# Kernel optimization log

Measured on AMD Instinct MI355X. Metric: run time of the kernel, lower is better.

The kernel has to match this reference:

```python
import jax, jax.numpy as jnp
import numpy as np

D_MODEL = 1024

def setup_inputs() -> dict:
    key = jax.random.key(0)
    ks = jax.random.split(key, 7)
    s = 1.0 / np.sqrt(D_MODEL)
    x = jax.random.normal(ks[0], (4, 2048, D_MODEL), dtype=jnp.float32)
    wq_w = jax.random.uniform(ks[1], (D_MODEL, D_MODEL), jnp.float32, -s, s)
    wq_b = jax.random.uniform(ks[2], (D_MODEL,), jnp.float32, -s, s)
    wk_w = jax.random.uniform(ks[3], (D_MODEL, D_MODEL), jnp.float32, -s, s)
    wk_b = jax.random.uniform(ks[4], (D_MODEL,), jnp.float32, -s, s)
    wv_w = jax.random.uniform(ks[5], (D_MODEL, D_MODEL), jnp.float32, -s, s)
    wv_b = jax.random.uniform(ks[6], (D_MODEL,), jnp.float32, -s, s)
    return {"x": x, "wq_w": wq_w, "wq_b": wq_b, "wk_w": wk_w, "wk_b": wk_b, "wv_w": wv_w, "wv_b": wv_b}

def reference(x, wq_w, wq_b, wk_w, wk_b, wv_w, wv_b):
    # Linear: x @ W^T + b (torch nn.Linear convention)
    q = jnp.einsum('bsd,ed->bse', x, wq_w) + wq_b
    k = jnp.einsum('bsd,ed->bse', x, wk_w) + wk_b
    v = jnp.einsum('bsd,ed->bse', x, wv_w) + wv_b
    scale = 1.0 / jnp.sqrt(jnp.asarray(k.shape[-1], dtype=q.dtype))
    logits = jnp.einsum('bqd,bkd->bqk', q, k) * scale  # [B, S, S]
    attn = jax.nn.softmax(logits, axis=-1)
    out = jnp.einsum('bqk,bkd->bqd', attn, v)
    return (attn, out)
```

## Files before the change

kernel.cpp:

```cpp
#include <hip/hip_runtime.h>

typedef unsigned short u16;
typedef u16 u16x4 __attribute__((ext_vector_type(4)));
typedef u16 u16x8 __attribute__((ext_vector_type(8)));
typedef __bf16 bf16x8 __attribute__((ext_vector_type(8)));
typedef float f32x4 __attribute__((ext_vector_type(4)));
typedef float f32x16 __attribute__((ext_vector_type(16)));

static __device__ __forceinline__ u16 f2bf(float f) {
  unsigned u = __builtin_bit_cast(unsigned, f);
  u += 0x7fffu + ((u >> 16) & 1u);
  return (u16)(u >> 16);
}
static __device__ __forceinline__ float bf2f(u16 h) {
  return __builtin_bit_cast(float, ((unsigned)h) << 16);
}

static __device__ __forceinline__ void gload_lds16(const u16* g, u16* l) {
  u16* gn = const_cast<u16*>(g);
  __builtin_amdgcn_global_load_lds(
      (__attribute__((address_space(1))) unsigned int*)gn,
      (__attribute__((address_space(3))) unsigned int*)l,
      16, 0, 0);
}

__global__ __launch_bounds__(256)
void cvt_f32_bf16(const float* __restrict__ in, u16* __restrict__ out) {
  const int i = blockIdx.x * 256 + threadIdx.x;
  float4 f = ((const float4*)in)[i];
  u16x4 o = { f2bf(f.x), f2bf(f.y), f2bf(f.z), f2bf(f.w) };
  ((u16x4*)out)[i] = o;
}

__global__ __launch_bounds__(256)
void cvt_w3(const float* __restrict__ a, const float* __restrict__ b,
            const float* __restrict__ c, u16* __restrict__ out) {
  const int blk = blockIdx.x;
  const int w = blk >> 10;
  const float* src = (w == 0) ? a : (w == 1) ? b : c;
  const int i = (blk & 1023) * 256 + threadIdx.x;
  float4 f = ((const float4*)src)[i];
  u16x4 o = { f2bf(f.x), f2bf(f.y), f2bf(f.z), f2bf(f.w) };
  ((u16x4*)(out + (size_t)w * 1048576ULL))[i] = o;
}


#define MM16(a, b, c) __builtin_amdgcn_mfma_f32_16x16x32_bf16(a, b, c, 0, 0, 0)

#define STAGE_A(BUF, J, KT) \
  gload_lds16(Ag + (size_t)(J) * 32 * lda + (KT), AsW + (BUF) * 16384 + (J) * 2048)
#define STAGE_B(BUF, KS, RH, KT) \
  gload_lds16(Bg + (size_t)(RH) * 32 * ldb + (KS) * 32 + (KT), \
              BsW + (BUF) * 16384 + (KS) * 2048 + (RH) * 1024)

#define APTR(BUF, MI, KS) \
  ((const bf16x8*)(ArdBase + (BUF) * 16384 + (MI) * 1024 + ((pA0 ^ ((KS) << 2)) << 3)))
#define BPTR(BUF, NI, KS) \
  ((const bf16x8*)(BrdBase + (BUF) * 16384 + (KS) * 2048 + (NI) * 512))

#define RD8(S, BUF, MH, KS) \
    S##A0 = *APTR(BUF, (MH) * 4 + 0, KS); \
    S##A1 = *APTR(BUF, (MH) * 4 + 1, KS); \
    S##A2 = *APTR(BUF, (MH) * 4 + 2, KS); \
    S##A3 = *APTR(BUF, (MH) * 4 + 3, KS); \
    S##B0 = *BPTR(BUF, 0, KS); \
    S##B1 = *BPTR(BUF, 1, KS); \
    S##B2 = *BPTR(BUF, 2, KS); \
    S##B3 = *BPTR(BUF, 3, KS)

#define PH(CUR, NXT, MH, NBUF, NMH, NKS, STG) do {                          \
    RD8(NXT, NBUF, NMH, NKS);                                               \
    STG;                                                                    \
    __builtin_amdgcn_s_barrier();                                           \
    asm volatile("s_waitcnt lgkmcnt(8)" ::: "memory");                      \
    __builtin_amdgcn_sched_barrier(0);                                      \
    __builtin_amdgcn_s_setprio(1);                                          \
    acc[(MH)*4+0][0] = MM16(CUR##A0, CUR##B0, acc[(MH)*4+0][0]);            \
    acc[(MH)*4+1][0] = MM16(CUR##A1, CUR##B0, acc[(MH)*4+1][0]);            \
    acc[(MH)*4+2][0] = MM16(CUR##A2, CUR##B0, acc[(MH)*4+2][0]);            \
    acc[(MH)*4+3][0] = MM16(CUR##A3, CUR##B0, acc[(MH)*4+3][0]);            \
    acc[(MH)*4+0][1] = MM16(CUR##A0, CUR##B1, acc[(MH)*4+0][1]);            \
    acc[(MH)*4+1][1] = MM16(CUR##A1, CUR##B1, acc[(MH)*4+1][1]);            \
    acc[(MH)*4+2][1] = MM16(CUR##A2, CUR##B1, acc[(MH)*4+2][1]);            \
    acc[(MH)*4+3][1] = MM16(CUR##A3, CUR##B1, acc[(MH)*4+3][1]);            \
    acc[(MH)*4+0][2] = MM16(CUR##A0, CUR##B2, acc[(MH)*4+0][2]);            \
    acc[(MH)*4+1][2] = MM16(CUR##A1, CUR##B2, acc[(MH)*4+1][2]);            \
    acc[(MH)*4+2][2] = MM16(CUR##A2, CUR##B2, acc[(MH)*4+2][2]);            \
    acc[(MH)*4+3][2] = MM16(CUR##A3, CUR##B2, acc[(MH)*4+3][2]);            \
    acc[(MH)*4+0][3] = MM16(CUR##A0, CUR##B3, acc[(MH)*4+0][3]);            \
    acc[(MH)*4+1][3] = MM16(CUR##A1, CUR##B3, acc[(MH)*4+1][3]);            \
    acc[(MH)*4+2][3] = MM16(CUR##A2, CUR##B3, acc[(MH)*4+2][3]);            \
    acc[(MH)*4+3][3] = MM16(CUR##A3, CUR##B3, acc[(MH)*4+3][3]);            \
    __builtin_amdgcn_s_setprio(0);                                          \
    asm volatile("s_waitcnt vmcnt(2)" ::: "memory");                        \
    __builtin_amdgcn_sched_barrier(0);                                      \
    __builtin_amdgcn_s_barrier();                                           \
  } while (0)

template<int MODE>
__global__ __launch_bounds__(512, 2)
void gemm8p(const u16* __restrict__ Ain, const u16* __restrict__ Bin,
            void* __restrict__ Cv,
            const float* __restrict__ b0, const float* __restrict__ b1,
            const float* __restrict__ b2,
            int lda, int ldb, int ldc, int K,
            unsigned long long sA, unsigned long long sB, unsigned long long sC,
            int nbx, int nby)
{
  __shared__ alignas(16) u16 As[2 * 2 * 128 * 64];
  __shared__ alignas(16) u16 Bs[2 * 4 * 2 * 64 * 32];

  const int nbxy = nbx * nby;
  const int bid  = blockIdx.x;
  const int flat = (bid & 7) * ((int)gridDim.x >> 3) + (bid >> 3);
  const int z    = flat / nbxy;
  const int rr   = flat - z * nbxy;
  const int width = nbx << 3;
  const int gid  = rr / width;
  const int rw   = rr - gid * width;
  const int by   = (gid << 3) + (rw & 7);
  const int bx   = rw >> 3;

  const u16* A = Ain + z * sA;
  const u16* B = Bin + z * sB;

  const int tid  = threadIdx.x;
  const int wave = tid >> 6;
  const int lane = tid & 63;
  const int wr   = wave >> 2;
  const int wc   = wave & 3;
  const int l16  = lane & 15;
  const int l4   = lane >> 4;

  const int m0 = by << 8;
  const int n0 = bx << 8;

  const int asr = wc * 8 + (lane >> 3);
  const int asc = ((lane & 7) ^ (lane >> 3)) << 3;
  const u16* Ag = A + (size_t)(m0 + wr * 128 + asr) * lda + asc;
  u16* AsW = As + wr * 8192 + wc * 512;

  const int bsr = wr * 16 + (lane >> 2);
  const int bsc = ((lane & 3) ^ ((lane >> 3) & 3)) << 3;
  const u16* Bg = B + (size_t)(n0 + wc * 64 + bsr) * ldb + bsc;
  u16* BsW = Bs + wc * 4096 + wr * 512;

  const u16* ArdBase = As + (wr * 128 + l16) * 64;
  const int pA0 = l4 ^ (l16 & 7);
  const u16* BrdBase = Bs + wc * 4096 + l16 * 32 + ((l4 ^ ((l16 >> 1) & 3)) << 3);

  f32x4 acc[8][4];
  #pragma unroll
  for (int i = 0; i < 8; ++i)
    #pragma unroll
    for (int j = 0; j < 4; ++j)
      #pragma unroll
      for (int r = 0; r < 4; ++r)
        acc[i][j][r] = 0.f;

  bf16x8 xA0, xA1, xA2, xA3, xB0, xB1, xB2, xB3;
  bf16x8 yA0, yA1, yA2, yA3, yB0, yB1, yB2, yB3;

  STAGE_A(0, 0, 0); STAGE_A(0, 1, 0);
  STAGE_B(0, 0, 0, 0); STAGE_B(0, 0, 1, 0);
  STAGE_B(0, 1, 0, 0); STAGE_B(0, 1, 1, 0);
  STAGE_A(0, 2, 0); STAGE_A(0, 3, 0);
  asm volatile("s_waitcnt vmcnt(0)" ::: "memory");
  __builtin_amdgcn_sched_barrier(0);
  __builtin_amdgcn_s_barrier();
  RD8(x, 0, 0, 0);

  const int NT = K >> 6;
  for (int t = 0; t < NT; t += 2) {
    const int k1 = (t + 1) * 64;
    const int k2 = (t + 2 < NT) ? (t + 2) * 64 : 0;
    PH(x, y, 0, 0, 0, 1, STAGE_A(1, 0, k1); STAGE_A(1, 1, k1));
    PH(y, x, 0, 0, 1, 0, STAGE_B(1, 0, 0, k1); STAGE_B(1, 0, 1, k1));
    PH(x, y, 1, 0, 1, 1, STAGE_B(1, 1, 0, k1); STAGE_B(1, 1, 1, k1));
    PH(y, x, 1, 1, 0, 0, STAGE_A(1, 2, k1); STAGE_A(1, 3, k1));
    PH(x, y, 0, 1, 0, 1, STAGE_A(0, 0, k2); STAGE_A(0, 1, k2));
    PH(y, x, 0, 1, 1, 0, STAGE_B(0, 0, 0, k2); STAGE_B(0, 0, 1, k2));
    PH(x, y, 1, 1, 1, 1, STAGE_B(0, 1, 0, k2); STAGE_B(0, 1, 1, k2));
    PH(y, x, 1, 0, 0, 0, STAGE_A(0, 2, k2); STAGE_A(0, 3, k2));
  }
  asm volatile("s_waitcnt vmcnt(0)" ::: "memory");

  if constexpr (MODE == 0) {
    const int g = n0 >> 10;
    const int colb = (n0 + wc * 64) & 1023;
    const int rowb = m0 + wr * 128 + l4 * 4;
    if (g < 2) {
      u16* Cb = (u16*)Cv + (size_t)g * 8388608ULL;
      const float* bp = (g == 0) ? b0 : b1;
      const float qs = (g == 0) ? 0.03125f : 1.0f;
      #pragma unroll
      for (int ni = 0; ni < 4; ++ni) {
        const int col = colb + ni * 16 + l16;
        const float bv = bp[col];
        #pragma unroll
        for (int mi = 0; mi < 8; ++mi) {
          const int row = rowb + mi * 16;
          #pragma unroll
          for (int r = 0; r < 4; ++r)
            Cb[(size_t)(row + r) * 1024 + col] = f2bf((acc[mi][ni][r] + bv) * qs);
        }
      }
    } else {
      u16* Vt = (u16*)Cv + 16777216ULL;
      #pragma unroll
      for (int ni = 0; ni < 4; ++ni) {
        const int col = colb + ni * 16 + l16;
        const float bv = b2[col];
        #pragma unroll
        for (int mi = 0; mi < 8; ++mi) {
          const int row = rowb + mi * 16;
          u16x4 o;
          #pragma unroll
          for (int r = 0; r < 4; ++r) o[r] = f2bf(acc[mi][ni][r] + bv);
          const size_t idx = ((size_t)((row >> 11) * 1024 + col)) * 2048 + (row & 2047);
          *(u16x4*)&Vt[idx] = o;
        }
      }
    }
  } else {
    u16* Cb = (u16*)Cv + (size_t)z * sC;
    #pragma unroll
    for (int ni = 0; ni < 4; ++ni) {
      const int col = n0 + wc * 64 + ni * 16 + l16;
      #pragma unroll
      for (int mi = 0; mi < 8; ++mi) {
        const int row = m0 + wr * 128 + mi * 16 + l4 * 4;
        #pragma unroll
        for (int r = 0; r < 4; ++r)
          Cb[(size_t)(row + r) * ldc + col] = f2bf(acc[mi][ni][r]);
      }
    }
  }
}

template<int MODE>
__global__ __launch_bounds__(256)
void gemm_bt(const u16* __restrict__ Ain, const u16* __restrict__ Bin,
             void* __restrict__ Cv,
             const float* __restrict__ b0, const float* __restrict__ b1,
             const float* __restrict__ b2,
             int lda, int ldb, int ldc, int K,
             unsigned long long sA, unsigned long long sB, unsigned long long sC,
             int nbx, int nby)
{
  constexpr int BM = 128, BN = 128, BK = 64;
  __shared__ alignas(16) u16 As[BM * BK];
  __shared__ alignas(16) u16 Bs[BN * BK];

  const int nbxy = nbx * nby;
  const int bid  = blockIdx.x;
  const int flat = (bid & 7) * ((int)gridDim.x >> 3) + (bid >> 3);
  const int z    = flat / nbxy;
  const int rr   = flat - z * nbxy;
  const int width = nbx << 3;
  const int gid  = rr / width;
  const int rw   = rr - gid * width;
  const int by   = (gid << 3) + (rw & 7);
  const int bx   = rw >> 3;

  const u16* A = Ain + z * sA;
  const u16* B = Bin + z * sB;

  const int tid  = threadIdx.x;
  const int wave = tid >> 6;
  const int lane = tid & 63;
  const int l32  = lane & 31;
  const int half = lane >> 5;
  const int wr   = wave >> 1;
  const int wc   = wave & 1;

  const int m0 = by * BM;
  const int n0 = bx * BN;

  const int lr = lane >> 3;
  const int sc = ((lane & 7) ^ lr) * 8;
  const u16* Ag = A + (size_t)(m0 + wave * 32 + lr) * lda + sc;
  const u16* Bg = B + (size_t)(n0 + wave * 32 + lr) * ldb + sc;
  u16* Asb = &As[(wave * 32) * BK];
  u16* Bsb = &Bs[(wave * 32) * BK];

  f32x16 acc[2][2];
  #pragma unroll
  for (int i = 0; i < 2; ++i)
    #pragma unroll
    for (int j = 0; j < 2; ++j)
      #pragma unroll
      for (int r = 0; r < 16; ++r)
        acc[i][j][r] = 0.f;

  for (int k0 = 0; k0 < K; k0 += BK) {
    gload_lds16(Ag + k0,                    Asb);
    gload_lds16(Ag + (size_t) 8 * lda + k0, Asb +  8 * BK);
    gload_lds16(Ag + (size_t)16 * lda + k0, Asb + 16 * BK);
    gload_lds16(Ag + (size_t)24 * lda + k0, Asb + 24 * BK);
    gload_lds16(Bg + k0,                    Bsb);
    gload_lds16(Bg + (size_t) 8 * ldb + k0, Bsb +  8 * BK);
    gload_lds16(Bg + (size_t)16 * ldb + k0, Bsb + 16 * BK);
    gload_lds16(Bg + (size_t)24 * ldb + k0, Bsb + 24 * BK);
    __syncthreads();

    #pragma unroll
    for (int ks = 0; ks < 4; ++ks) {
      bf16x8 af[2], bfr[2];
      #pragma unroll
      for (int ti = 0; ti < 2; ++ti) {
        const int row = wr * 64 + ti * 32 + l32;
        const int ch  = ((ks * 2 + half) ^ (row & 7)) * 8;
        af[ti] = *(const bf16x8*)&As[row * BK + ch];
      }
      #pragma unroll
      for (int tj = 0; tj < 2; ++tj) {
        const int row = wc * 64 + tj * 32 + l32;
        const int ch  = ((ks * 2 + half) ^ (row & 7)) * 8;
        bfr[tj] = *(const bf16x8*)&Bs[row * BK + ch];
      }
      #pragma unroll
      for (int ti = 0; ti < 2; ++ti)
        #pragma unroll
        for (int tj = 0; tj < 2; ++tj)
          acc[ti][tj] = __builtin_amdgcn_mfma_f32_32x32x16_bf16(af[ti], bfr[tj], acc[ti][tj], 0, 0, 0);
    }
    __syncthreads();
  }

  const int colb = n0 + wc * 64 + l32;
  const int rowb = m0 + wr * 64 + 4 * half;

  if constexpr (MODE == 3) {
    float* Cf = (float*)Cv + z * sC;
    #pragma unroll
    for (int tj = 0; tj < 2; ++tj) {
      const int col = colb + tj * 32;
      #pragma unroll
      for (int ti = 0; ti < 2; ++ti)
        #pragma unroll
        for (int g4 = 0; g4 < 4; ++g4)
          #pragma unroll
          for (int r = 0; r < 4; ++r) {
            const int row = rowb + ti * 32 + g4 * 8 + r;
            Cf[(size_t)row * ldc + col] = acc[ti][tj][g4 * 4 + r];
          }
    }
  }
}

__global__ __launch_bounds__(256)
void softmax_rows(u16* __restrict__ logits, float* __restrict__ attn) {
  const int row = blockIdx.x;
  const int tid = threadIdx.x;
  u16*   lp = logits + (size_t)row * 2048 + tid * 8;
  float* ap = attn   + (size_t)row * 2048 + tid * 8;

  u16x8 raw = *(const u16x8*)lp;
  float v[8];
  #pragma unroll
  for (int j = 0; j < 8; ++j) v[j] = bf2f(raw[j]);

  float mx = v[0];
  #pragma unroll
  for (int j = 1; j < 8; ++j) mx = fmaxf(mx, v[j]);
  #pragma unroll
  for (int o = 32; o > 0; o >>= 1) mx = fmaxf(mx, __shfl_xor(mx, o, 64));

  __shared__ float smax[4], ssum[4];
  const int wv = tid >> 6, ln = tid & 63;
  if (ln == 0) smax[wv] = mx;
  __syncthreads();
  mx = fmaxf(fmaxf(smax[0], smax[1]), fmaxf(smax[2], smax[3]));

  float s = 0.f;
  #pragma unroll
  for (int j = 0; j < 8; ++j) { v[j] = __expf(v[j] - mx); s += v[j]; }
  #pragma unroll
  for (int o = 32; o > 0; o >>= 1) s += __shfl_xor(s, o, 64);
  if (ln == 0) ssum[wv] = s;
  __syncthreads();
  s = (ssum[0] + ssum[1]) + (ssum[2] + ssum[3]);
  const float inv = 1.f / s;

  u16x8 ob;
  #pragma unroll
  for (int j = 0; j < 8; ++j) { v[j] *= inv; ob[j] = f2bf(v[j]); }
  float4* apv = (float4*)ap;
  apv[0] = make_float4(v[0], v[1], v[2], v[3]);
  apv[1] = make_float4(v[4], v[5], v[6], v[7]);
  *(u16x8*)lp = ob;
}

extern "C" void kernel_launch(void* const* d_in, const int* in_sizes, int n_in,
                              void* d_out, int out_size, void* d_ws, size_t ws_size,
                              hipStream_t stream) {
  (void)in_sizes; (void)n_in; (void)out_size; (void)ws_size;
  const float* x    = (const float*)d_in[0];
  const float* wq_w = (const float*)d_in[1];
  const float* wq_b = (const float*)d_in[2];
  const float* wk_w = (const float*)d_in[3];
  const float* wk_b = (const float*)d_in[4];
  const float* wv_w = (const float*)d_in[5];
  const float* wv_b = (const float*)d_in[6];

  float* attn = (float*)d_out;
  float* outp = attn + 16777216ULL;

  u16* xb   = (u16*)d_ws;
  u16* wcat = xb   + 8388608ULL;
  u16* Qb   = wcat + 3145728ULL;
  u16* Kb   = Qb   + 8388608ULL;
  u16* Vt   = Kb   + 8388608ULL;
  u16* Lg   = Vt   + 8388608ULL;

  cvt_f32_bf16<<<8192, 256, 0, stream>>>(x, xb);
  cvt_w3<<<3072, 256, 0, stream>>>(wq_w, wk_w, wv_w, wcat);

  gemm8p<0><<<384, 512, 0, stream>>>(xb, wcat, Qb, wq_b, wk_b, wv_b,
                                     1024, 1024, 1024, 1024, 0, 0, 0, 12, 32);

  gemm8p<2><<<256, 512, 0, stream>>>(Qb, Kb, Lg, nullptr, nullptr, nullptr,
                                     1024, 1024, 2048, 1024,
                                     2097152ULL, 2097152ULL, 4194304ULL, 8, 8);

  softmax_rows<<<8192, 256, 0, stream>>>(Lg, attn);

  gemm_bt<3><<<512, 256, 0, stream>>>(Lg, Vt, outp, nullptr, nullptr, nullptr,
                                      2048, 2048, 1024, 2048,
                                      4194304ULL, 2097152ULL, 2097152ULL, 8, 16);
}
```

Before: 332.0 us.

## Restructure gemm8p LDS staging into k-half tiles with deeper prefetch and B-register reuse

Reworks the 256x256 GEMM pipeline. Shared-memory tiles are now split into two 32-wide k-halves for both A and B, with a single swizzle pattern. Loads are issued one k-tile further ahead, with vmcnt waits only every fourth phase, and B fragments are read once and reused across the two M-halves instead of being re-read per phase. The cost is waiting for all LDS reads (lgkmcnt(0)) before each MFMA batch, which drops the previous register double-buffering, and launch bounds drop to one block per CU. The gemm_bt signature also loses its unused bias pointers.

```diff
diff --git a/kernel.cpp b/kernel.cpp
--- a/kernel.cpp
+++ b/kernel.cpp
@@ -47,58 +47,67 @@
 
 #define MM16(a, b, c) __builtin_amdgcn_mfma_f32_16x16x32_bf16(a, b, c, 0, 0, 0)
 
-#define STAGE_A(BUF, J, KT) \
-  gload_lds16(Ag + (size_t)(J) * 32 * lda + (KT), AsW + (BUF) * 16384 + (J) * 2048)
-#define STAGE_B(BUF, KS, RH, KT) \
-  gload_lds16(Bg + (size_t)(RH) * 32 * ldb + (KS) * 32 + (KT), \
-              BsW + (BUF) * 16384 + (KS) * 2048 + (RH) * 1024)
+#define STAGE_A(BUF, KH, KT) do {                                            \
+    gload_lds16(Asrc + (KT) + (KH) * 32,                                     \
+                AsW + (BUF) * 16384 + (KH) * 8192);                          \
+    gload_lds16(Asrc + (size_t)128 * lda + (KT) + (KH) * 32,                 \
+                AsW + (BUF) * 16384 + (KH) * 8192 + 4096);                   \
+  } while (0)
+#define STAGE_B(BUF, KH, KT) do {                                            \
+    gload_lds16(Bsrc + (KT) + (KH) * 32,                                     \
+                BsW + (BUF) * 16384 + (KH) * 8192);                          \
+    gload_lds16(Bsrc + (size_t)128 * ldb + (KT) + (KH) * 32,                 \
+                BsW + (BUF) * 16384 + (KH) * 8192 + 4096);                   \
+  } while (0)
 
 #define APTR(BUF, MI, KS) \
-  ((const bf16x8*)(ArdBase + (BUF) * 16384 + (MI) * 1024 + ((pA0 ^ ((KS) << 2)) << 3)))
+  ((const bf16x8*)(ArdBase + (BUF) * 16384 + (KS) * 8192 + (MI) * 512))
 #define BPTR(BUF, NI, KS) \
-  ((const bf16x8*)(BrdBase + (BUF) * 16384 + (KS) * 2048 + (NI) * 512))
-
-#define RD8(S, BUF, MH, KS) \
-    S##A0 = *APTR(BUF, (MH) * 4 + 0, KS); \
-    S##A1 = *APTR(BUF, (MH) * 4 + 1, KS); \
-    S##A2 = *APTR(BUF, (MH) * 4 + 2, KS); \
-    S##A3 = *APTR(BUF, (MH) * 4 + 3, KS); \
-    S##B0 = *BPTR(BUF, 0, KS); \
-    S##B1 = *BPTR(BUF, 1, KS); \
-    S##B2 = *BPTR(BUF, 2, KS); \
-    S##B3 = *BPTR(BUF, 3, KS)
-
-#define PH(CUR, NXT, MH, NBUF, NMH, NKS, STG) do {                          \
-    RD8(NXT, NBUF, NMH, NKS);                                               \
-    STG;                                                                    \
-    __builtin_amdgcn_s_barrier();                                           \
-    asm volatile("s_waitcnt lgkmcnt(8)" ::: "memory");                      \
-    __builtin_amdgcn_sched_barrier(0);                                      \
-    __builtin_amdgcn_s_setprio(1);                                          \
-    acc[(MH)*4+0][0] = MM16(CUR##A0, CUR##B0, acc[(MH)*4+0][0]);            \
-    acc[(MH)*4+1][0] = MM16(CUR##A1, CUR##B0, acc[(MH)*4+1][0]);            \
-    acc[(MH)*4+2][0] = MM16(CUR##A2, CUR##B0, acc[(MH)*4+2][0]);            \
-    acc[(MH)*4+3][0] = MM16(CUR##A3, CUR##B0, acc[(MH)*4+3][0]);            \
-    acc[(MH)*4+0][1] = MM16(CUR##A0, CUR##B1, acc[(MH)*4+0][1]);            \
-    acc[(MH)*4+1][1] = MM16(CUR##A1, CUR##B1, acc[(MH)*4+1][1]);            \
-    acc[(MH)*4+2][1] = MM16(CUR##A2, CUR##B1, acc[(MH)*4+2][1]);            \
-    acc[(MH)*4+3][1] = MM16(CUR##A3, CUR##B1, acc[(MH)*4+3][1]);            \
-    acc[(MH)*4+0][2] = MM16(CUR##A0, CUR##B2, acc[(MH)*4+0][2]);            \
-    acc[(MH)*4+1][2] = MM16(CUR##A1, CUR##B2, acc[(MH)*4+1][2]);            \
-    acc[(MH)*4+2][2] = MM16(CUR##A2, CUR##B2, acc[(MH)*4+2][2]);            \
-    acc[(MH)*4+3][2] = MM16(CUR##A3, CUR##B2, acc[(MH)*4+3][2]);            \
-    acc[(MH)*4+0][3] = MM16(CUR##A0, CUR##B3, acc[(MH)*4+0][3]);            \
-    acc[(MH)*4+1][3] = MM16(CUR##A1, CUR##B3, acc[(MH)*4+1][3]);            \
-    acc[(MH)*4+2][3] = MM16(CUR##A2, CUR##B3, acc[(MH)*4+2][3]);            \
-    acc[(MH)*4+3][3] = MM16(CUR##A3, CUR##B3, acc[(MH)*4+3][3]);            \
-    __builtin_amdgcn_s_setprio(0);                                          \
-    asm volatile("s_waitcnt vmcnt(2)" ::: "memory");                        \
-    __builtin_amdgcn_sched_barrier(0);                                      \
-    __builtin_amdgcn_s_barrier();                                           \
+  ((const bf16x8*)(BrdBase + (BUF) * 16384 + (KS) * 8192 + (NI) * 512))
+
+#define VM4   asm volatile("s_waitcnt vmcnt(4)" ::: "memory")
+#define NOVM  (void)0
+
+#define PH(BUF, MH, KS, RDB, STG, VMW) do {                                  \
+    bf16x8 a0 = *APTR(BUF, (MH) * 4 + 0, KS);                                \
+    bf16x8 a1 = *APTR(BUF, (MH) * 4 + 1, KS);                                \
+    bf16x8 a2 = *APTR(BUF, (MH) * 4 + 2, KS);                                \
+    bf16x8 a3 = *APTR(BUF, (MH) * 4 + 3, KS);                                \
+    if (RDB) {                                                               \
+      bf0 = *BPTR(BUF, 0, KS);                                               \
+      bf1 = *BPTR(BUF, 1, KS);                                               \
+      bf2 = *BPTR(BUF, 2, KS);                                               \
+      bf3 = *BPTR(BUF, 3, KS);                                               \
+    }                                                                        \
+    STG;                                                                     \
+    __builtin_amdgcn_s_barrier();                                            \
+    asm volatile("s_waitcnt lgkmcnt(0)" ::: "memory");                       \
+    __builtin_amdgcn_sched_barrier(0);                                       \
+    __builtin_amdgcn_s_setprio(1);                                           \
+    acc[(MH)*4+0][0] = MM16(a0, bf0, acc[(MH)*4+0][0]);                      \
+    acc[(MH)*4+1][0] = MM16(a1, bf0, acc[(MH)*4+1][0]);                      \
+    acc[(MH)*4+2][0] = MM16(a2, bf0, acc[(MH)*4+2][0]);                      \
+    acc[(MH)*4+3][0] = MM16(a3, bf0, acc[(MH)*4+3][0]);                      \
+    acc[(MH)*4+0][1] = MM16(a0, bf1, acc[(MH)*4+0][1]);                      \
+    acc[(MH)*4+1][1] = MM16(a1, bf1, acc[(MH)*4+1][1]);                      \
+    acc[(MH)*4+2][1] = MM16(a2, bf1, acc[(MH)*4+2][1]);                      \
+    acc[(MH)*4+3][1] = MM16(a3, bf1, acc[(MH)*4+3][1]);                      \
+    acc[(MH)*4+0][2] = MM16(a0, bf2, acc[(MH)*4+0][2]);                      \
+    acc[(MH)*4+1][2] = MM16(a1, bf2, acc[(MH)*4+1][2]);                      \
+    acc[(MH)*4+2][2] = MM16(a2, bf2, acc[(MH)*4+2][2]);                      \
+    acc[(MH)*4+3][2] = MM16(a3, bf2, acc[(MH)*4+3][2]);                      \
+    acc[(MH)*4+0][3] = MM16(a0, bf3, acc[(MH)*4+0][3]);                      \
+    acc[(MH)*4+1][3] = MM16(a1, bf3, acc[(MH)*4+1][3]);                      \
+    acc[(MH)*4+2][3] = MM16(a2, bf3, acc[(MH)*4+2][3]);                      \
+    acc[(MH)*4+3][3] = MM16(a3, bf3, acc[(MH)*4+3][3]);                      \
+    __builtin_amdgcn_s_setprio(0);                                           \
+    VMW;                                                                     \
+    __builtin_amdgcn_sched_barrier(0);                                       \
+    __builtin_amdgcn_s_barrier();                                            \
   } while (0)
 
 template<int MODE>
-__global__ __launch_bounds__(512, 2)
+__global__ __launch_bounds__(512, 1)
 void gemm8p(const u16* __restrict__ Ain, const u16* __restrict__ Bin,
             void* __restrict__ Cv,
             const float* __restrict__ b0, const float* __restrict__ b1,
@@ -107,8 +116,8 @@
             unsigned long long sA, unsigned long long sB, unsigned long long sC,
             int nbx, int nby)
 {
-  __shared__ alignas(16) u16 As[2 * 2 * 128 * 64];
-  __shared__ alignas(16) u16 Bs[2 * 4 * 2 * 64 * 32];
+  __shared__ alignas(16) u16 As[2 * 2 * 256 * 32];
+  __shared__ alignas(16) u16 Bs[2 * 2 * 256 * 32];
 
   const int nbxy = nbx * nby;
   const int bid  = blockIdx.x;
@@ -135,19 +144,15 @@
   const int m0 = by << 8;
   const int n0 = bx << 8;
 
-  const int asr = wc * 8 + (lane >> 3);
-  const int asc = ((lane & 7) ^ (lane >> 3)) << 3;
-  const u16* Ag = A + (size_t)(m0 + wr * 128 + asr) * lda + asc;
-  u16* AsW = As + wr * 8192 + wc * 512;
-
-  const int bsr = wr * 16 + (lane >> 2);
-  const int bsc = ((lane & 3) ^ ((lane >> 3) & 3)) << 3;
-  const u16* Bg = B + (size_t)(n0 + wc * 64 + bsr) * ldb + bsc;
-  u16* BsW = Bs + wc * 4096 + wr * 512;
-
-  const u16* ArdBase = As + (wr * 128 + l16) * 64;
-  const int pA0 = l4 ^ (l16 & 7);
-  const u16* BrdBase = Bs + wc * 4096 + l16 * 32 + ((l4 ^ ((l16 >> 1) & 3)) << 3);
+  const int gch = (tid & 3) ^ ((tid >> 3) & 3);
+  const u16* Asrc = A + (size_t)(m0 + (tid >> 2)) * lda + gch * 8;
+  const u16* Bsrc = B + (size_t)(n0 + (tid >> 2)) * ldb + gch * 8;
+  u16* AsW = As + tid * 8;
+  u16* BsW = Bs + tid * 8;
+
+  const int rsw = (l4 ^ ((l16 >> 1) & 3)) << 3;
+  const u16* ArdBase = As + (size_t)(wr * 128 + l16) * 32 + rsw;
+  const u16* BrdBase = Bs + (size_t)(wc * 64 + l16) * 32 + rsw;
 
   f32x4 acc[8][4];
   #pragma unroll
@@ -158,30 +163,28 @@
       for (int r = 0; r < 4; ++r)
         acc[i][j][r] = 0.f;
 
-  bf16x8 xA0, xA1, xA2, xA3, xB0, xB1, xB2, xB3;
-  bf16x8 yA0, yA1, yA2, yA3, yB0, yB1, yB2, yB3;
-
-  STAGE_A(0, 0, 0); STAGE_A(0, 1, 0);
-  STAGE_B(0, 0, 0, 0); STAGE_B(0, 0, 1, 0);
-  STAGE_B(0, 1, 0, 0); STAGE_B(0, 1, 1, 0);
-  STAGE_A(0, 2, 0); STAGE_A(0, 3, 0);
-  asm volatile("s_waitcnt vmcnt(0)" ::: "memory");
+  bf16x8 bf0, bf1, bf2, bf3;
+
+  STAGE_A(0, 0, 0);  STAGE_B(0, 0, 0);
+  STAGE_A(0, 1, 0);  STAGE_B(0, 1, 0);
+  STAGE_A(1, 0, 64); STAGE_B(1, 0, 64);
+  VM4;
   __builtin_amdgcn_sched_barrier(0);
   __builtin_amdgcn_s_barrier();
-  RD8(x, 0, 0, 0);
 
   const int NT = K >> 6;
   for (int t = 0; t < NT; t += 2) {
-    const int k1 = (t + 1) * 64;
-    const int k2 = (t + 2 < NT) ? (t + 2) * 64 : 0;
-    PH(x, y, 0, 0, 0, 1, STAGE_A(1, 0, k1); STAGE_A(1, 1, k1));
-    PH(y, x, 0, 0, 1, 0, STAGE_B(1, 0, 0, k1); STAGE_B(1, 0, 1, k1));
-    PH(x, y, 1, 0, 1, 1, STAGE_B(1, 1, 0, k1); STAGE_B(1, 1, 1, k1));
-    PH(y, x, 1, 1, 0, 0, STAGE_A(1, 2, k1); STAGE_A(1, 3, k1));
-    PH(x, y, 0, 1, 0, 1, STAGE_A(0, 0, k2); STAGE_A(0, 1, k2));
-    PH(y, x, 0, 1, 1, 0, STAGE_B(0, 0, 0, k2); STAGE_B(0, 0, 1, k2));
-    PH(x, y, 1, 1, 1, 1, STAGE_B(0, 1, 0, k2); STAGE_B(0, 1, 1, k2));
-    PH(y, x, 1, 0, 0, 0, STAGE_A(0, 2, k2); STAGE_A(0, 3, k2));
+    const int kt1 = (t + 1) * 64;
+    const int kt2 = (t + 2 < NT) ? (t + 2) * 64 : 0;
+    const int kt3 = (t + 3 < NT) ? (t + 3) * 64 : 0;
+    PH(0, 0, 0, 1, STAGE_A(1, 1, kt1), NOVM);
+    PH(0, 1, 0, 0, STAGE_B(1, 1, kt1), NOVM);
+    PH(0, 0, 1, 1, STAGE_A(0, 0, kt2), NOVM);
+    PH(0, 1, 1, 0, STAGE_B(0, 0, kt2), VM4);
+    PH(1, 0, 0, 1, STAGE_A(0, 1, kt2), NOVM);
+    PH(1, 1, 0, 0, STAGE_B(0, 1, kt2), NOVM);
+    PH(1, 0, 1, 1, STAGE_A(1, 0, kt3), NOVM);
+    PH(1, 1, 1, 0, STAGE_B(1, 0, kt3), VM4);
   }
   asm volatile("s_waitcnt vmcnt(0)" ::: "memory");
 
@@ -242,15 +245,13 @@
 __global__ __launch_bounds__(256)
 void gemm_bt(const u16* __restrict__ Ain, const u16* __restrict__ Bin,
              void* __restrict__ Cv,
-             const float* __restrict__ b0, const float* __restrict__ b1,
-             const float* __restrict__ b2,
              int lda, int ldb, int ldc, int K,
              unsigned long long sA, unsigned long long sB, unsigned long long sC,
              int nbx, int nby)
 {
-  constexpr int BM = 128, BN = 128, BK = 64;
+  constexpr int BM = 128, BK = 64;
   __shared__ alignas(16) u16 As[BM * BK];
-  __shared__ alignas(16) u16 Bs[BN * BK];
+  __shared__ alignas(16) u16 Bs[BM * BK];
 
   const int nbxy = nbx * nby;
   const int bid  = blockIdx.x;
@@ -275,7 +276,7 @@
   const int wc   = wave & 1;
 
   const int m0 = by * BM;
-  const int n0 = bx * BN;
+  const int n0 = bx * BM;
 
   const int lr = lane >> 3;
   const int sc = ((lane & 7) ^ lr) * 8;
@@ -426,7 +427,7 @@
 
   softmax_rows<<<8192, 256, 0, stream>>>(Lg, attn);
 
-  gemm_bt<3><<<512, 256, 0, stream>>>(Lg, Vt, outp, nullptr, nullptr, nullptr,
+  gemm_bt<3><<<512, 256, 0, stream>>>(Lg, Vt, outp,
                                       2048, 2048, 1024, 2048,
                                       4194304ULL, 2097152ULL, 2097152ULL, 8, 16);
 }
```

After: 314.2 us. 1.06x faster.
